# Performance work log

Hardware: AMD Instinct MI355X
Metric: run time of the kernel (lower is better)

Reference implementation:

```python
import jax, jax.numpy as jnp
import numpy as np

N = 100000   # nodes
E = 400000   # edges
G = 1024     # graphs in batch
IN = 4; H = 128; HD = 4; DH = H // HD; L = 3; ED = 4; FF = 2 * H; JK = H * L
SCALE = 1.0 / np.sqrt(DH).astype(np.float32)


def _ln(x, g, b):
    m = x.mean(-1, keepdims=True)
    v = x.var(-1, keepdims=True)
    return (x - m) / jnp.sqrt(v + 1e-5) * g + b


def setup_inputs() -> dict:
    key = jax.random.key(0)
    ks = jax.random.split(key, 24)
    rn = lambda k, s, sc=0.05: jax.random.normal(k, s, jnp.float32) * sc
    return {
        "x": rn(ks[0], (N, IN), 1.0),
        "edge_index": jax.random.randint(ks[1], (2, E), 0, N),
        "edge_attr": rn(ks[2], (E, ED), 1.0),
        "batch": jnp.sort(jax.random.randint(ks[3], (N,), 0, G)),
        "u": rn(ks[4], (G, 1), 1.0),
        "Win": rn(ks[5], (IN, H)), "b_in": jnp.zeros(H),
        "Wq": rn(ks[6], (L, H, H)), "bq": jnp.zeros((L, H)),
        "Wk": rn(ks[7], (L, H, H)), "bk": jnp.zeros((L, H)),
        "Wv": rn(ks[8], (L, H, H)), "bv": jnp.zeros((L, H)),
        "We": rn(ks[9], (L, ED, H)),
        "Wskip": rn(ks[10], (L, H, H)), "bskip": jnp.zeros((L, H)),
        "ln1_g": jnp.ones((L, H)), "ln1_b": jnp.zeros((L, H)),
        "Wf1": rn(ks[11], (L, H, FF)), "bf1": jnp.zeros((L, FF)),
        "Wf2": rn(ks[12], (L, FF, H)), "bf2": jnp.zeros((L, H)),
        "ln2_g": jnp.ones((L, H)), "ln2_b": jnp.zeros((L, H)),
        "Wg1": rn(ks[13], (JK, H)), "bg1": jnp.zeros(H),
        "Wg2": rn(ks[14], (H, 1)), "bg2": jnp.zeros(1),
        "Wh1": rn(ks[15], (JK + 1, H)), "bh1": jnp.zeros(H),
        "Wh2": rn(ks[16], (H, 3)), "bh2": jnp.zeros(3),
    }


def reference(x, edge_index, edge_attr, batch, u,
              Win, b_in, Wq, bq, Wk, bk, Wv, bv, We, Wskip, bskip,
              ln1_g, ln1_b, Wf1, bf1, Wf2, bf2, ln2_g, ln2_b,
              Wg1, bg1, Wg2, bg2, Wh1, bh1, Wh2, bh2):
    src, dst = edge_index[0], edge_index[1]
    h = x @ Win + b_in                                   # [N,H]
    xs = []
    for l in range(L):
        q = (h @ Wq[l] + bq[l]).reshape(N, HD, DH)
        k_n = h @ Wk[l] + bk[l]
        v_n = h @ Wv[l] + bv[l]
        e = edge_attr @ We[l]                            # [E,H] edge bias
        ke = (k_n[src] + e).reshape(E, HD, DH)
        ve = (v_n[src] + e).reshape(E, HD, DH)
        logits = (q[dst] * ke).sum(-1) * SCALE           # [E,HD]
        m = jax.ops.segment_max(logits, dst, N)
        p = jnp.exp(logits - m[dst])
        s = jax.ops.segment_sum(p, dst, N)
        alpha = p / (s[dst] + 1e-16)                     # segment softmax per dst node
        agg = jax.ops.segment_sum(alpha[:, :, None] * ve, dst, N).reshape(N, H)
        attn = agg + h @ Wskip[l] + bskip[l]             # root weight (skip lin)
        h = _ln(h + attn, ln1_g[l], ln1_b[l])
        ff = jax.nn.relu(h @ Wf1[l] + bf1[l]) @ Wf2[l] + bf2[l]
        h = _ln(h + ff, ln2_g[l], ln2_b[l])
        xs.append(h)
    xc = jnp.concatenate(xs, -1)                         # JumpingKnowledge 'cat' [N,JK]
    gate = (jax.nn.relu(xc @ Wg1 + bg1) @ Wg2 + bg2)[:, 0]  # [N]
    gm = jax.ops.segment_max(gate, batch, G)
    gp = jnp.exp(gate - gm[batch])
    gs = jax.ops.segment_sum(gp, batch, G)
    w = gp / (gs[batch] + 1e-16)                         # per-graph softmax
    pooled = jax.ops.segment_sum(w[:, None] * xc, batch, G)  # [G,JK]
    out = jnp.concatenate([pooled, u], 1)                # [G,JK+1]
    return jax.nn.relu(out @ Wh1 + bh1) @ Wh2 + bh2      # [G,3]
```

## Files before the change

kernel.cpp:

```cpp
#include <hip/hip_runtime.h>
#include <math.h>

#define H 128
#define LAYERS 3
#define FFDIM 256
#define JK 384
#define ATT_SCALE 0.17677669529663687f

typedef unsigned short u16;
typedef __attribute__((ext_vector_type(4))) float f32x4;
typedef __attribute__((ext_vector_type(8))) short short8;
typedef __attribute__((ext_vector_type(8))) unsigned short ushort8v;

static inline int cdiv(int a, int b) { return (a + b - 1) / b; }

static __device__ __forceinline__ float bf2f(u16 u) {
    union { unsigned int i; float f; } v; v.i = ((unsigned int)u) << 16; return v.f;
}
static __device__ __forceinline__ u16 f2bf(float f) {
    union { float f; unsigned int i; } v; v.f = f;
    unsigned int r = v.i + 0x7FFFu + ((v.i >> 16) & 1u);
    return (u16)(r >> 16);
}

__global__ void hist_kernel(const int* __restrict__ ei, int* __restrict__ counts, int E) {
    int e = blockIdx.x * blockDim.x + threadIdx.x;
    if (e >= E) return;
    atomicAdd(&counts[ei[E + e]], 1);
}

__global__ __launch_bounds__(256) void scan1_kernel(const int* __restrict__ counts,
                                                    int* __restrict__ offsets,
                                                    int* __restrict__ bsum, int N) {
    __shared__ int sh[256];
    int t = threadIdx.x;
    int base = blockIdx.x * 1024 + t * 4;
    int v0 = 0, v1 = 0, v2 = 0, v3 = 0;
    if (base + 3 < N) {
        int4 q = *(const int4*)&counts[base];
        v0 = q.x; v1 = q.y; v2 = q.z; v3 = q.w;
    } else {
        if (base < N) v0 = counts[base];
        if (base + 1 < N) v1 = counts[base + 1];
        if (base + 2 < N) v2 = counts[base + 2];
        if (base + 3 < N) v3 = counts[base + 3];
    }
    int ts = v0 + v1 + v2 + v3;
    sh[t] = ts; __syncthreads();
    for (int off = 1; off < 256; off <<= 1) {
        int x = (t >= off) ? sh[t - off] : 0;
        __syncthreads(); sh[t] += x; __syncthreads();
    }
    int excl = sh[t] - ts;
    if (base < N)     offsets[base]     = excl;
    if (base + 1 < N) offsets[base + 1] = excl + v0;
    if (base + 2 < N) offsets[base + 2] = excl + v0 + v1;
    if (base + 3 < N) offsets[base + 3] = excl + v0 + v1 + v2;
    if (t == 255) bsum[blockIdx.x] = sh[255];
}

__global__ __launch_bounds__(128) void scan2_kernel(const int* __restrict__ bsum,
                                                    int* __restrict__ boffs,
                                                    int* __restrict__ offsets, int nb, int N) {
    __shared__ int sh[128];
    int t = threadIdx.x;
    int s = (t < nb) ? bsum[t] : 0;
    sh[t] = s; __syncthreads();
    for (int off = 1; off < 128; off <<= 1) {
        int x = (t >= off) ? sh[t - off] : 0;
        __syncthreads(); sh[t] += x; __syncthreads();
    }
    if (t < nb) boffs[t] = sh[t] - s;
    if (t == 0) offsets[N] = sh[nb - 1];
}

__global__ __launch_bounds__(256) void scan3_kernel(int* __restrict__ offsets,
                                                    const int* __restrict__ boffs, int N) {
    int add = boffs[blockIdx.x];
    int base = blockIdx.x * 1024 + threadIdx.x * 4;
#pragma unroll
    for (int i = 0; i < 4; ++i)
        if (base + i < N) offsets[base + i] += add;
}

__global__ void scatter_kernel(const int* __restrict__ ei, const float* __restrict__ eattr,
                               const int* __restrict__ offsets,
                               int* __restrict__ cursor, int* __restrict__ psrc,
                               float4* __restrict__ pe, int E) {
    int e = blockIdx.x * blockDim.x + threadIdx.x;
    if (e >= E) return;
    int d = ei[E + e];
    int pos = atomicAdd(&cursor[d], 1);
    int o = offsets[d] + pos;
    psrc[o] = ei[e];
    pe[o] = *(const float4*)&eattr[(size_t)e * 4];
}

__global__ __launch_bounds__(256) void dhist_kernel(const int* __restrict__ counts,
                                                    int* __restrict__ dhist, int N) {
    __shared__ int lh[64];
    int t = threadIdx.x;
    if (t < 64) lh[t] = 0;
    __syncthreads();
    int n = blockIdx.x * 256 + t;
    if (n < N) atomicAdd(&lh[min(counts[n], 63)], 1);
    __syncthreads();
    if (t < 64 && lh[t]) atomicAdd(&dhist[t], lh[t]);
}

__global__ __launch_bounds__(64) void dscan_kernel(const int* __restrict__ dhist,
                                                   int* __restrict__ dcur) {
    __shared__ int sh[64];
    int t = threadIdx.x;
    int s = dhist[t];
    sh[t] = s; __syncthreads();
    for (int off = 1; off < 64; off <<= 1) {
        int x = (t >= off) ? sh[t - off] : 0;
        __syncthreads(); sh[t] += x; __syncthreads();
    }
    dcur[t] = sh[t] - s;
}

__global__ __launch_bounds__(256) void dscatter_kernel(const int* __restrict__ counts,
                                                       int* __restrict__ dcur,
                                                       int* __restrict__ nperm, int N) {
    __shared__ int lh[64], lbase[64];
    int t = threadIdx.x;
    if (t < 64) lh[t] = 0;
    __syncthreads();
    int n = blockIdx.x * 256 + t;
    int b = 0, rank = 0;
    if (n < N) {
        b = min(counts[n], 63);
        rank = atomicAdd(&lh[b], 1);
    }
    __syncthreads();
    if (t < 64 && lh[t]) lbase[t] = atomicAdd(&dcur[t], lh[t]);
    __syncthreads();
    if (n < N) nperm[lbase[b] + rank] = n;
}

__global__ void graph_bounds_kernel(const int* __restrict__ batch, int* __restrict__ gstart,
                                    int N, int G) {
    int g = blockIdx.x * blockDim.x + threadIdx.x;
    if (g > G) return;
    int lo = 0, hi = N;
    while (lo < hi) { int mid = (lo + hi) >> 1; if (batch[mid] < g) lo = mid + 1; else hi = mid; }
    gstart[g] = lo;
}

struct TD { const float* src; int dstoff, K, N; };
struct TA { TD d[19]; };

__global__ __launch_bounds__(256) void wconv_kernel(TA a, u16* __restrict__ WT) {
    TD d = a.d[blockIdx.y];
    int i = blockIdx.x * 256 + threadIdx.x;
    int tot = d.K * d.N;
    if (i >= tot) return;
    int c = i / d.K, k = i - c * d.K;
    WT[d.dstoff + i] = f2bf(d.src[(size_t)k * d.N + c]);
}

__global__ __launch_bounds__(256) void input_proj_kernel(const float* __restrict__ x,
                                                         const float* __restrict__ Win,
                                                         const float* __restrict__ b_in,
                                                         u16* __restrict__ h, int ldh, int N) {
    int idx = blockIdx.x * 256 + threadIdx.x;
    int n = idx >> 6, c = (idx & 63) * 2;
    if (n >= N) return;
    float4 xv = *(const float4*)&x[(size_t)n * 4];
    float o0 = b_in[c]     + xv.x * Win[c]     + xv.y * Win[H + c]     + xv.z * Win[2 * H + c]     + xv.w * Win[3 * H + c];
    float o1 = b_in[c + 1] + xv.x * Win[c + 1] + xv.y * Win[H + c + 1] + xv.z * Win[2 * H + c + 1] + xv.w * Win[3 * H + c + 1];
    ushort2 s; s.x = f2bf(o0); s.y = f2bf(o1);
    *(ushort2*)&h[(size_t)n * ldh + c] = s;
}

__device__ __forceinline__ void stage_tile(const u16* __restrict__ g, int ld, int row0,
                                           int nrows, int kt, u16* __restrict__ sm, int t) {
#pragma unroll
    for (int i = 0; i < 4; ++i) {
        int f = i * 256 + t;
        int row = f >> 3, ck = f & 7;
        int n = row0 + row; if (n >= nrows) n = nrows - 1;
        uint4 v = *(const uint4*)(g + (size_t)n * ld + kt + ck * 8);
        int sw = ck ^ (row & 7);
        *(uint4*)(sm + row * 64 + sw * 8) = v;
    }
}

template <int MODE, int NBY>
__global__ __launch_bounds__(256) void gemm_mfma(
    const u16* __restrict__ A, int lda,
    const u16* __restrict__ WT, int K,
    const float* __restrict__ b0, const float* __restrict__ b1,
    const float* __restrict__ b2, const float* __restrict__ b3,
    const u16* __restrict__ resid16,
    u16* __restrict__ obf, u16* __restrict__ obf2, float* __restrict__ of32,
    int nrows)
{
    alignas(16) __shared__ char smemraw[33792];
    u16* Asm = (u16*)smemraw;
    u16* Bsm = (u16*)(smemraw + 16384);
    float* stage = (float*)smemraw;
    int t = threadIdx.x;
    int lane = t & 63, wid = t >> 6;
    int wr = wid >> 1, wc = wid & 1;

    int T = gridDim.x, id = blockIdx.x;
    int qd = T >> 3, rr = T & 7;
    int xcd = id & 7, pos = id >> 3;
    int swz = (xcd < rr ? xcd * (qd + 1) : rr * (qd + 1) + (xcd - rr) * qd) + pos;
    int by = swz & (NBY - 1);
    int row0 = (swz / NBY) * 128;

    const u16* WTb = WT + (size_t)by * 128 * K;

    f32x4 acc[4][4] = {};

    for (int kt = 0; kt < K; kt += 64) {
        stage_tile(A, lda, row0, nrows, kt, Asm, t);
        stage_tile(WTb, K, 0, 128, kt, Bsm, t);
        __syncthreads();
        int g = lane >> 4;
        int l15 = lane & 15;
#pragma unroll
        for (int kk = 0; kk < 2; ++kk) {
            int cb = kk * 4 + g;
            short8 af[4], bf[4];
#pragma unroll
            for (int mi = 0; mi < 4; ++mi) {
                int r = wr * 64 + mi * 16 + l15;
                af[mi] = *(const short8*)(Asm + r * 64 + ((cb ^ (r & 7)) * 8));
            }
#pragma unroll
            for (int nj = 0; nj < 4; ++nj) {
                int c = wc * 64 + nj * 16 + l15;
                bf[nj] = *(const short8*)(Bsm + c * 64 + ((cb ^ (c & 7)) * 8));
            }
#pragma unroll
            for (int mi = 0; mi < 4; ++mi)
#pragma unroll
                for (int nj = 0; nj < 4; ++nj)
                    acc[mi][nj] = __builtin_amdgcn_mfma_f32_16x16x32_bf16(af[mi], bf[nj], acc[mi][nj], 0, 0, 0);
        }
        __syncthreads();
    }

    int g = lane >> 4, l15 = lane & 15;

    if (MODE == 3) {
        float* gsum = (float*)Asm;
        float part[4][4];
#pragma unroll
        for (int mi = 0; mi < 4; ++mi)
#pragma unroll
            for (int r = 0; r < 4; ++r) part[mi][r] = 0.f;
#pragma unroll
        for (int nj = 0; nj < 4; ++nj) {
            int col = wc * 64 + nj * 16 + l15;
            float bb = b0[col];
            float w2 = b1[col];
#pragma unroll
            for (int mi = 0; mi < 4; ++mi)
#pragma unroll
                for (int r = 0; r < 4; ++r) {
                    float v = fmaxf(acc[mi][nj][r] + bb, 0.f);
                    part[mi][r] = fmaf(v, w2, part[mi][r]);
                }
        }
#pragma unroll
        for (int off = 1; off <= 8; off <<= 1)
#pragma unroll
            for (int mi = 0; mi < 4; ++mi)
#pragma unroll
                for (int r = 0; r < 4; ++r) part[mi][r] += __shfl_xor(part[mi][r], off);
        if (wc == 0 && l15 == 0) {
#pragma unroll
            for (int mi = 0; mi < 4; ++mi)
#pragma unroll
                for (int r = 0; r < 4; ++r)
                    gsum[wr * 64 + mi * 16 + g * 4 + r] = part[mi][r];
        }
        __syncthreads();
        if (wc == 1 && l15 == 0) {
            float bg2v = b2[0];
#pragma unroll
            for (int mi = 0; mi < 4; ++mi)
#pragma unroll
                for (int r = 0; r < 4; ++r) {
                    int lr = wr * 64 + mi * 16 + g * 4 + r;
                    int n = row0 + lr;
                    if (n < nrows) of32[n] = part[mi][r] + gsum[lr] + bg2v;
                }
        }
        return;
    }

    const float* bias;
    u16* ob = nullptr; int ldob = 384;
    if (MODE == 0) {
        bias = (by == 0) ? b0 : (by == 1) ? b1 : (by == 2) ? b2 : b3;
        if (by < 3) ob = obf + by * 128;
        else { ob = obf2; ldob = 128; }
    } else if (MODE == 1) {
        bias = b0 + by * 128;
        ob = obf + by * 128;
    } else {
        bias = b0;
        ob = obf;
    }

#pragma unroll
    for (int p = 0; p < 2; ++p) {
        if (wr == p) {
#pragma unroll
            for (int nj = 0; nj < 4; ++nj) {
                int col = wc * 64 + nj * 16 + l15;
                float bb = bias[col];
#pragma unroll
                for (int mi = 0; mi < 4; ++mi)
#pragma unroll
                    for (int r = 0; r < 4; ++r) {
                        float v = acc[mi][nj][r] + bb;
                        if (MODE == 1) v = fmaxf(v, 0.f);
                        stage[(mi * 16 + g * 4 + r) * 132 + col] = v;
                    }
            }
        }
        __syncthreads();
        if (MODE == 2) {
            int sub2 = t & 15, rowg = t >> 4;
#pragma unroll
            for (int it = 0; it < 4; ++it) {
                int lr = it * 16 + rowg;
                int gr = row0 + p * 64 + lr;
                bool ok = gr < nrows;
                int c8 = sub2 * 8;
                float tv[8]; float sum = 0.f, sq = 0.f;
                if (ok) {
                    ushort8v rv = *(const ushort8v*)&resid16[(size_t)gr * 384 + c8];
#pragma unroll
                    for (int i = 0; i < 8; ++i) {
                        tv[i] = stage[lr * 132 + c8 + i] + bf2f(rv[i]);
                        sum += tv[i]; sq += tv[i] * tv[i];
                    }
                }
#pragma unroll
                for (int off = 1; off <= 8; off <<= 1) { sum += __shfl_xor(sum, off); sq += __shfl_xor(sq, off); }
                if (ok) {
                    float mean = sum * (1.f / 128.f);
                    float var = sq * (1.f / 128.f) - mean * mean;
                    float rstd = rsqrtf(var + 1e-5f);
                    ushort8v o;
#pragma unroll
                    for (int i = 0; i < 8; ++i)
                        o[i] = f2bf((tv[i] - mean) * rstd * b1[c8 + i] + b2[c8 + i]);
                    *(ushort8v*)&ob[(size_t)gr * 384 + c8] = o;
                }
            }
        } else {
#pragma unroll
            for (int it = 0; it < 4; ++it) {
                int lr = it * 16 + (t >> 4);
                int gr = row0 + p * 64 + lr;
                if (gr < nrows) {
                    int c8 = (t & 15) * 8;
                    ushort8v o;
                    if (MODE == 0 && by == 3) {
                        ushort8v hv = *(const ushort8v*)&A[(size_t)gr * lda + c8];
#pragma unroll
                        for (int i = 0; i < 8; ++i) o[i] = f2bf(stage[lr * 132 + c8 + i] + bf2f(hv[i]));
                    } else {
#pragma unroll
                        for (int i = 0; i < 8; ++i) o[i] = f2bf(stage[lr * 132 + c8 + i]);
                    }
                    *(ushort8v*)&ob[(size_t)gr * ldob + c8] = o;
                }
            }
        }
        __syncthreads();
    }
}

__global__ __launch_bounds__(256) void attn_kernel(
    u16* __restrict__ qkv,
    const u16* __restrict__ skipb,
    const int* __restrict__ offsets,
    const int* __restrict__ nperm,
    const int* __restrict__ psrc, const float4* __restrict__ pe,
    const float* __restrict__ We_l,
    const float* __restrict__ g1, const float* __restrict__ b1,
    int N)
{
    int tid = threadIdx.x;
    int grp = tid >> 4;
    int sub = tid & 15;
    int idx = blockIdx.x * 16 + grp;
    if (idx >= N) return;
    int n = nperm[idx];
    int d0 = sub * 8;

    float we[4][8];
#pragma unroll
    for (int aa = 0; aa < 4; ++aa) {
        float4 w0 = *(const float4*)&We_l[aa * H + d0];
        float4 w1 = *(const float4*)&We_l[aa * H + d0 + 4];
        we[aa][0] = w0.x; we[aa][1] = w0.y; we[aa][2] = w0.z; we[aa][3] = w0.w;
        we[aa][4] = w1.x; we[aa][5] = w1.y; we[aa][6] = w1.z; we[aa][7] = w1.w;
    }

    ushort8v qraw = *(const ushort8v*)&qkv[(size_t)n * JK + d0];
    float qf[8];
#pragma unroll
    for (int i = 0; i < 8; ++i) qf[i] = bf2f(qraw[i]);

    float qe[4];
#pragma unroll
    for (int aa = 0; aa < 4; ++aa) {
        float s = 0.f;
#pragma unroll
        for (int i = 0; i < 8; ++i) s = fmaf(qf[i], we[aa][i], s);
        s += __shfl_xor(s, 1);
        s += __shfl_xor(s, 2);
        qe[aa] = s;
    }

    float m0 = -INFINITY, ss0 = 0.f, m1 = -INFINITY, ss1 = 0.f;
    float a0[8] = {}, a1[8] = {};
    float w0a = 0.f, w0b = 0.f, w0c = 0.f, w0d = 0.f;
    float w1a = 0.f, w1b = 0.f, w1c = 0.f, w1d = 0.f;
    int e0v = offsets[n], e1v = offsets[n + 1];
    int deg = e1v - e0v;
    int npairs = deg >> 1;

    if (npairs > 0) {
        int j0 = e0v;
        int sA = psrc[j0], sB = psrc[j0 + 1];
        float4 eaA = pe[j0], eaB = pe[j0 + 1];
        const u16* srA = qkv + (size_t)sA * JK;
        const u16* srB = qkv + (size_t)sB * JK;
        ushort8v krA = *(const ushort8v*)&srA[H + d0];
        ushort8v vrA = *(const ushort8v*)&srA[2 * H + d0];
        ushort8v krB = *(const ushort8v*)&srB[H + d0];
        ushort8v vrB = *(const ushort8v*)&srB[2 * H + d0];
        for (int it = 0; it < npairs; ++it) {
            float4 eaA2, eaB2; ushort8v krA2, vrA2, krB2, vrB2;
            if (it + 1 < npairs) {
                int jn = e0v + (it + 1) * 2;
                int sA2 = psrc[jn], sB2 = psrc[jn + 1];
                eaA2 = pe[jn]; eaB2 = pe[jn + 1];
                const u16* srA2 = qkv + (size_t)sA2 * JK;
                const u16* srB2 = qkv + (size_t)sB2 * JK;
                krA2 = *(const ushort8v*)&srA2[H + d0];
                vrA2 = *(const ushort8v*)&srA2[2 * H + d0];
                krB2 = *(const ushort8v*)&srB2[H + d0];
                vrB2 = *(const ushort8v*)&srB2[2 * H + d0];
            }
            float pA = 0.f, pB = 0.f;
#pragma unroll
            for (int i = 0; i < 8; ++i) {
                pA = fmaf(qf[i], bf2f(krA[i]), pA);
                pB = fmaf(qf[i], bf2f(krB[i]), pB);
            }
            pA += __shfl_xor(pA, 1); pB += __shfl_xor(pB, 1);
            pA += __shfl_xor(pA, 2); pB += __shfl_xor(pB, 2);
            float lgA = (pA + eaA.x * qe[0] + eaA.y * qe[1] + eaA.z * qe[2] + eaA.w * qe[3]) * ATT_SCALE;
            float lgB = (pB + eaB.x * qe[0] + eaB.y * qe[1] + eaB.z * qe[2] + eaB.w * qe[3]) * ATT_SCALE;
            float mnA = fmaxf(m0, lgA);
            float mnB = fmaxf(m1, lgB);
            float cA = __expf(m0 - mnA), cB = __expf(m1 - mnB);
            float pvA = __expf(lgA - mnA), pvB = __expf(lgB - mnB);
            ss0 = ss0 * cA + pvA;
            ss1 = ss1 * cB + pvB;
#pragma unroll
            for (int i = 0; i < 8; ++i) {
                a0[i] = a0[i] * cA + pvA * bf2f(vrA[i]);
                a1[i] = a1[i] * cB + pvB * bf2f(vrB[i]);
            }
            w0a = w0a * cA + pvA * eaA.x; w0b = w0b * cA + pvA * eaA.y;
            w0c = w0c * cA + pvA * eaA.z; w0d = w0d * cA + pvA * eaA.w;
            w1a = w1a * cB + pvB * eaB.x; w1b = w1b * cB + pvB * eaB.y;
            w1c = w1c * cB + pvB * eaB.z; w1d = w1d * cB + pvB * eaB.w;
            m0 = mnA; m1 = mnB;
            krA = krA2; vrA = vrA2; eaA = eaA2;
            krB = krB2; vrB = vrB2; eaB = eaB2;
        }
    }
    if (deg & 1) {
        int j = e1v - 1;
        int s = psrc[j];
        float4 ea = pe[j];
        const u16* sr = qkv + (size_t)s * JK;
        ushort8v kr = *(const ushort8v*)&sr[H + d0];
        ushort8v vr = *(const ushort8v*)&sr[2 * H + d0];
        float part = 0.f;
#pragma unroll
        for (int i = 0; i < 8; ++i) part = fmaf(qf[i], bf2f(kr[i]), part);
        part += __shfl_xor(part, 1);
        part += __shfl_xor(part, 2);
        float lg = (part + ea.x * qe[0] + ea.y * qe[1] + ea.z * qe[2] + ea.w * qe[3]) * ATT_SCALE;
        float mn = fmaxf(m0, lg);
        float c = __expf(m0 - mn);
        float pv = __expf(lg - mn);
        ss0 = ss0 * c + pv;
#pragma unroll
        for (int i = 0; i < 8; ++i) a0[i] = a0[i] * c + pv * bf2f(vr[i]);
        w0a = w0a * c + pv * ea.x; w0b = w0b * c + pv * ea.y;
        w0c = w0c * c + pv * ea.z; w0d = w0d * c + pv * ea.w;
        m0 = mn;
    }
    float mm = fmaxf(m0, m1);
    if (mm > -INFINITY) {
        float c0 = (m0 > -INFINITY) ? __expf(m0 - mm) : 0.f;
        float c1 = (m1 > -INFINITY) ? __expf(m1 - mm) : 0.f;
        ss0 = ss0 * c0 + ss1 * c1;
#pragma unroll
        for (int i = 0; i < 8; ++i) a0[i] = a0[i] * c0 + a1[i] * c1;
        w0a = w0a * c0 + w1a * c1; w0b = w0b * c0 + w1b * c1;
        w0c = w0c * c0 + w1c * c1; w0d = w0d * c0 + w1d * c1;
    }
    float inv = 1.f / (ss0 + 1e-16f);
#pragma unroll
    for (int i = 0; i < 8; ++i)
        a0[i] += w0a * we[0][i] + w0b * we[1][i] + w0c * we[2][i] + w0d * we[3][i];

    ushort8v skraw = *(const ushort8v*)&skipb[(size_t)n * H + d0];
    float tv[8], sum = 0.f, sq = 0.f;
#pragma unroll
    for (int i = 0; i < 8; ++i) {
        tv[i] = a0[i] * inv + bf2f(skraw[i]);
        sum += tv[i]; sq += tv[i] * tv[i];
    }
#pragma unroll
    for (int off = 1; off <= 8; off <<= 1) { sum += __shfl_xor(sum, off); sq += __shfl_xor(sq, off); }
    float mean = sum * (1.f / 128.f);
    float var = sq * (1.f / 128.f) - mean * mean;
    float rstd = rsqrtf(var + 1e-5f);
    float4 ga = *(const float4*)&g1[d0];
    float4 gb = *(const float4*)&g1[d0 + 4];
    float4 ba = *(const float4*)&b1[d0];
    float4 bb = *(const float4*)&b1[d0 + 4];
    float gg[8] = {ga.x, ga.y, ga.z, ga.w, gb.x, gb.y, gb.z, gb.w};
    float bbv[8] = {ba.x, ba.y, ba.z, ba.w, bb.x, bb.y, bb.z, bb.w};
    ushort8v obv;
#pragma unroll
    for (int i = 0; i < 8; ++i)
        obv[i] = f2bf((tv[i] - mean) * rstd * gg[i] + bbv[i]);
    *(ushort8v*)&qkv[(size_t)n * JK + d0] = obv;
}

#define PCH 512
__global__ __launch_bounds__(256) void pool_kernel(const float* __restrict__ gate,
                                                   const u16* __restrict__ xc,
                                                   const int* __restrict__ gstart,
                                                   const float* __restrict__ u,
                                                   float* __restrict__ pooled, int G) {
    int g = blockIdx.x;
    int t = threadIdx.x;
    int s0 = gstart[g], s1 = gstart[g + 1];
    __shared__ float red[256];
    __shared__ float w[PCH];
    float mx = -INFINITY;
    for (int i = s0 + t; i < s1; i += 256) mx = fmaxf(mx, gate[i]);
    red[t] = mx; __syncthreads();
    for (int off = 128; off; off >>= 1) { if (t < off) red[t] = fmaxf(red[t], red[t + off]); __syncthreads(); }
    float gm = red[0]; __syncthreads();
    float sm = 0.f;
    for (int i = s0 + t; i < s1; i += 256) sm += __expf(gate[i] - gm);
    red[t] = sm; __syncthreads();
    for (int off = 128; off; off >>= 1) { if (t < off) red[t] += red[t + off]; __syncthreads(); }
    float inv = 1.f / (red[0] + 1e-16f);
    float acc0 = 0.f, acc1 = 0.f;
    for (int base = s0; base < s1; base += PCH) {
        int cnt = min(PCH, s1 - base);
        __syncthreads();
        for (int i = t; i < cnt; i += 256) w[i] = __expf(gate[base + i] - gm) * inv;
        __syncthreads();
        for (int c = 0; c < cnt; ++c) {
            const u16* row = xc + (size_t)(base + c) * JK;
            float wc = w[c];
            acc0 = fmaf(wc, bf2f(row[t]), acc0);
            if (t < 128) acc1 = fmaf(wc, bf2f(row[t + 256]), acc1);
        }
    }
    pooled[(size_t)g * (JK + 1) + t] = acc0;
    if (t < 128) pooled[(size_t)g * (JK + 1) + t + 256] = acc1;
    if (t == 0) pooled[(size_t)g * (JK + 1) + JK] = u[g];
}

__global__ __launch_bounds__(128) void head_kernel(const float* __restrict__ pooled,
                                                   const float* __restrict__ Wh1,
                                                   const float* __restrict__ bh1,
                                                   const float* __restrict__ Wh2,
                                                   const float* __restrict__ bh2,
                                                   float* __restrict__ out, int G) {
    int g = blockIdx.x;
    int j = threadIdx.x;
    __shared__ float hid[128];
    float acc = bh1[j];
    const float* pr = pooled + (size_t)g * (JK + 1);
    for (int k = 0; k < JK + 1; ++k) acc = fmaf(pr[k], Wh1[(size_t)k * H + j], acc);
    hid[j] = fmaxf(acc, 0.f);
    __syncthreads();
    if (j < 3) {
        float o = bh2[j];
        for (int k = 0; k < H; ++k) o += hid[k] * Wh2[k * 3 + j];
        out[(size_t)g * 3 + j] = o;
    }
}

extern "C" void kernel_launch(void* const* d_in, const int* in_sizes, int n_in,
                              void* d_out, int out_size, void* d_ws, size_t ws_size,
                              hipStream_t stream) {
    const float* x     = (const float*)d_in[0];
    const int*   ei    = (const int*)d_in[1];
    const float* eattr = (const float*)d_in[2];
    const int*   batch = (const int*)d_in[3];
    const float* u     = (const float*)d_in[4];
    const float* Win   = (const float*)d_in[5];
    const float* b_in  = (const float*)d_in[6];
    const float* Wq    = (const float*)d_in[7];
    const float* bq    = (const float*)d_in[8];
    const float* Wk    = (const float*)d_in[9];
    const float* bk    = (const float*)d_in[10];
    const float* Wv    = (const float*)d_in[11];
    const float* bv    = (const float*)d_in[12];
    const float* We    = (const float*)d_in[13];
    const float* Wskip = (const float*)d_in[14];
    const float* bskip = (const float*)d_in[15];
    const float* ln1_g = (const float*)d_in[16];
    const float* ln1_b = (const float*)d_in[17];
    const float* Wf1   = (const float*)d_in[18];
    const float* bf1   = (const float*)d_in[19];
    const float* Wf2   = (const float*)d_in[20];
    const float* bf2   = (const float*)d_in[21];
    const float* ln2_g = (const float*)d_in[22];
    const float* ln2_b = (const float*)d_in[23];
    const float* Wg1   = (const float*)d_in[24];
    const float* bg1   = (const float*)d_in[25];
    const float* Wg2   = (const float*)d_in[26];
    const float* bg2   = (const float*)d_in[27];
    const float* Wh1   = (const float*)d_in[28];
    const float* bh1   = (const float*)d_in[29];
    const float* Wh2   = (const float*)d_in[30];
    const float* bh2   = (const float*)d_in[31];

    const int N = in_sizes[3];
    const int E = in_sizes[1] / 2;
    const int G = in_sizes[4];

    char* p = (char*)d_ws;
    auto alloc = [&](size_t bytes) { char* r = p; p += (bytes + 255) & ~(size_t)255; return r; };
    int*    counts  = (int*)alloc((size_t)N * 4);
    int*    cursor  = (int*)alloc((size_t)N * 4);
    int*    offsets = (int*)alloc((size_t)(N + 1) * 4);
    int*    psrc    = (int*)alloc((size_t)E * 4);
    float4* pe      = (float4*)alloc((size_t)E * 16);
    int*    nperm   = (int*)alloc((size_t)N * 4);
    int*    gstart  = (int*)alloc((size_t)(G + 1) * 4);
    int*    bsum    = (int*)alloc(128 * 4);
    int*    boffs   = (int*)alloc(128 * 4);
    int*    dhist   = (int*)alloc(64 * 4);
    int*    dcur    = (int*)alloc(64 * 4);
    float*  gate    = (float*)alloc((size_t)N * 4);
    float*  pooled  = (float*)alloc((size_t)G * (JK + 1) * 4);
    u16*    WT      = (u16*)alloc((size_t)442368 * 2);
    u16*    skipb   = (u16*)alloc((size_t)N * H * 2);
    u16*    xc      = (u16*)alloc((size_t)N * JK * 2);
    u16*    qkv     = (u16*)alloc((size_t)N * JK * 2);

    const int QKVS_OFF = 0;
    const int F1_OFF   = 3 * 65536;
    const int F2_OFF   = F1_OFF + 3 * 32768;
    const int G1_OFF   = F2_OFF + 3 * 32768;

    hipMemsetAsync(counts, 0, (size_t)N * 4, stream);
    hipMemsetAsync(cursor, 0, (size_t)N * 4, stream);
    hipMemsetAsync(dhist, 0, 64 * 4, stream);

    int eb = cdiv(E, 256);
    int nb = cdiv(N, 1024);
    int nthb = cdiv(N, 256);
    hist_kernel<<<eb, 256, 0, stream>>>(ei, counts, E);
    scan1_kernel<<<nb, 256, 0, stream>>>(counts, offsets, bsum, N);
    scan2_kernel<<<1, 128, 0, stream>>>(bsum, boffs, offsets, nb, N);
    scan3_kernel<<<nb, 256, 0, stream>>>(offsets, boffs, N);
    scatter_kernel<<<eb, 256, 0, stream>>>(ei, eattr, offsets, cursor, psrc, pe, E);
    dhist_kernel<<<nthb, 256, 0, stream>>>(counts, dhist, N);
    dscan_kernel<<<1, 64, 0, stream>>>(dhist, dcur);
    dscatter_kernel<<<nthb, 256, 0, stream>>>(counts, dcur, nperm, N);
    graph_bounds_kernel<<<cdiv(G + 1, 256), 256, 0, stream>>>(batch, gstart, N, G);

    TA ta;
    for (int l = 0; l < 3; ++l) {
        ta.d[l * 4 + 0] = { Wq    + (size_t)l * 16384, QKVS_OFF + l * 65536 + 0,     128, 128 };
        ta.d[l * 4 + 1] = { Wk    + (size_t)l * 16384, QKVS_OFF + l * 65536 + 16384, 128, 128 };
        ta.d[l * 4 + 2] = { Wv    + (size_t)l * 16384, QKVS_OFF + l * 65536 + 32768, 128, 128 };
        ta.d[l * 4 + 3] = { Wskip + (size_t)l * 16384, QKVS_OFF + l * 65536 + 49152, 128, 128 };
        ta.d[12 + l]    = { Wf1   + (size_t)l * 32768, F1_OFF   + l * 32768,         128, 256 };
        ta.d[15 + l]    = { Wf2   + (size_t)l * 32768, F2_OFF   + l * 32768,         256, 128 };
    }
    ta.d[18] = { Wg1, G1_OFF, 384, 128 };
    dim3 wg(cdiv(49152, 256), 19);
    wconv_kernel<<<wg, 256, 0, stream>>>(ta, WT);

    input_proj_kernel<<<cdiv(N * 64, 256), 256, 0, stream>>>(x, Win, b_in, xc, JK, N);

    int gb = cdiv(N, 128);
    int nb16 = cdiv(N, 16);
    for (int l = 0; l < LAYERS; ++l) {
        const u16* hin = xc + (size_t)((l == 0) ? 0 : (l - 1) * H);
        gemm_mfma<0, 4><<<gb * 4, 256, 0, stream>>>(
            hin, JK, WT + QKVS_OFF + (size_t)l * 65536, 128,
            bq + l * H, bk + l * H, bv + l * H, bskip + l * H,
            nullptr, qkv, skipb, nullptr, N);
        attn_kernel<<<nb16, 256, 0, stream>>>(qkv, skipb, offsets, nperm, psrc, pe,
                                              We + (size_t)l * 4 * H, ln1_g + l * H, ln1_b + l * H,
                                              N);
        gemm_mfma<1, 2><<<gb * 2, 256, 0, stream>>>(
            qkv, JK, WT + F1_OFF + (size_t)l * 32768, 128,
            bf1 + (size_t)l * FFDIM, nullptr, nullptr, nullptr,
            nullptr, qkv + H, nullptr, nullptr, N);
        gemm_mfma<2, 1><<<gb, 256, 0, stream>>>(
            qkv + H, JK, WT + F2_OFF + (size_t)l * 32768, 256,
            bf2 + (size_t)l * H, ln2_g + (size_t)l * H, ln2_b + (size_t)l * H, nullptr,
            qkv, xc + (size_t)l * H, nullptr, nullptr, N);
    }

    gemm_mfma<3, 1><<<gb, 256, 0, stream>>>(
        xc, JK, WT + G1_OFF, JK,
        bg1, Wg2, bg2, nullptr,
        nullptr, nullptr, nullptr, gate, N);
    pool_kernel<<<G, 256, 0, stream>>>(gate, xc, gstart, u, pooled, G);
    head_kernel<<<G, 128, 0, stream>>>(pooled, Wh1, bh1, Wh2, bh2, (float*)d_out, G);
}
```

Measured before the change: 660.5 us.

## Fuse FFN two GEMMs, ReLU and LayerNorm into one kernel per layer

Replaces the separate FF1 (ReLU) and FF2 (+residual LayerNorm) GEMM launches with a single ff_fused kernel that processes 64-row tiles. The 256-wide hidden activation stays in swizzled shared memory instead of being written to and reread from global memory. The generic GEMM kernel loses its MODE 1/2 epilogues. In exchange the fused kernel uses about 56KB of LDS and smaller row tiles, which may lower occupancy, and it reloads the weights for every 64-row block.

```diff
diff --git a/kernel.cpp b/kernel.cpp
--- a/kernel.cpp
+++ b/kernel.cpp
@@ -194,7 +194,6 @@
     const u16* __restrict__ WT, int K,
     const float* __restrict__ b0, const float* __restrict__ b1,
     const float* __restrict__ b2, const float* __restrict__ b3,
-    const u16* __restrict__ resid16,
     u16* __restrict__ obf, u16* __restrict__ obf2, float* __restrict__ of32,
     int nrows)
 {
@@ -296,19 +295,10 @@
         return;
     }
 
-    const float* bias;
-    u16* ob = nullptr; int ldob = 384;
-    if (MODE == 0) {
-        bias = (by == 0) ? b0 : (by == 1) ? b1 : (by == 2) ? b2 : b3;
-        if (by < 3) ob = obf + by * 128;
-        else { ob = obf2; ldob = 128; }
-    } else if (MODE == 1) {
-        bias = b0 + by * 128;
-        ob = obf + by * 128;
-    } else {
-        bias = b0;
-        ob = obf;
-    }
+    const float* bias = (by == 0) ? b0 : (by == 1) ? b1 : (by == 2) ? b2 : b3;
+    u16* ob; int ldob;
+    if (by < 3) { ob = obf + by * 128; ldob = 384; }
+    else { ob = obf2; ldob = 128; }
 
 #pragma unroll
     for (int p = 0; p < 2; ++p) {
@@ -320,65 +310,193 @@
 #pragma unroll
                 for (int mi = 0; mi < 4; ++mi)
 #pragma unroll
-                    for (int r = 0; r < 4; ++r) {
-                        float v = acc[mi][nj][r] + bb;
-                        if (MODE == 1) v = fmaxf(v, 0.f);
-                        stage[(mi * 16 + g * 4 + r) * 132 + col] = v;
-                    }
+                    for (int r = 0; r < 4; ++r)
+                        stage[(mi * 16 + g * 4 + r) * 132 + col] = acc[mi][nj][r] + bb;
             }
         }
         __syncthreads();
-        if (MODE == 2) {
-            int sub2 = t & 15, rowg = t >> 4;
-#pragma unroll
-            for (int it = 0; it < 4; ++it) {
-                int lr = it * 16 + rowg;
-                int gr = row0 + p * 64 + lr;
-                bool ok = gr < nrows;
-                int c8 = sub2 * 8;
-                float tv[8]; float sum = 0.f, sq = 0.f;
-                if (ok) {
-                    ushort8v rv = *(const ushort8v*)&resid16[(size_t)gr * 384 + c8];
-#pragma unroll
-                    for (int i = 0; i < 8; ++i) {
-                        tv[i] = stage[lr * 132 + c8 + i] + bf2f(rv[i]);
-                        sum += tv[i]; sq += tv[i] * tv[i];
-                    }
+#pragma unroll
+        for (int it = 0; it < 4; ++it) {
+            int lr = it * 16 + (t >> 4);
+            int gr = row0 + p * 64 + lr;
+            if (gr < nrows) {
+                int c8 = (t & 15) * 8;
+                ushort8v o;
+                if (by == 3) {
+                    ushort8v hv = *(const ushort8v*)&A[(size_t)gr * lda + c8];
+#pragma unroll
+                    for (int i = 0; i < 8; ++i) o[i] = f2bf(stage[lr * 132 + c8 + i] + bf2f(hv[i]));
+                } else {
+#pragma unroll
+                    for (int i = 0; i < 8; ++i) o[i] = f2bf(stage[lr * 132 + c8 + i]);
                 }
-#pragma unroll
-                for (int off = 1; off <= 8; off <<= 1) { sum += __shfl_xor(sum, off); sq += __shfl_xor(sq, off); }
-                if (ok) {
-                    float mean = sum * (1.f / 128.f);
-                    float var = sq * (1.f / 128.f) - mean * mean;
-                    float rstd = rsqrtf(var + 1e-5f);
-                    ushort8v o;
-#pragma unroll
-                    for (int i = 0; i < 8; ++i)
-                        o[i] = f2bf((tv[i] - mean) * rstd * b1[c8 + i] + b2[c8 + i]);
-                    *(ushort8v*)&ob[(size_t)gr * 384 + c8] = o;
+                *(ushort8v*)&ob[(size_t)gr * ldob + c8] = o;
+            }
+        }
+        __syncthreads();
+    }
+}
+
+__global__ __launch_bounds__(256) void ff_fused(
+    const u16* __restrict__ qkv,
+    const u16* __restrict__ W1T,
+    const u16* __restrict__ W2T,
+    const float* __restrict__ bias1,
+    const float* __restrict__ bias2,
+    const float* __restrict__ g2, const float* __restrict__ b2v,
+    u16* __restrict__ xcout,
+    int nrows)
+{
+    alignas(16) __shared__ char smem[57344];
+    u16* ff1s = (u16*)smem;
+    u16* ast  = (u16*)(smem + 32768);
+    u16* bst  = (u16*)(smem + 40960);
+    float* stage = (float*)smem;
+
+    int t = threadIdx.x;
+    int lane = t & 63, wid = t >> 6;
+    int wr = wid >> 1, wc = wid & 1;
+    int g = lane >> 4, l15 = lane & 15;
+
+    int T = gridDim.x, id = blockIdx.x;
+    int qd = T >> 3, rr = T & 7;
+    int xcd = id & 7, pos = id >> 3;
+    int swz = (xcd < rr ? xcd * (qd + 1) : rr * (qd + 1) + (xcd - rr) * qd) + pos;
+    int row0 = swz * 64;
+
+    for (int ch = 0; ch < 2; ++ch) {
+        f32x4 acc[2][4] = {};
+        for (int kt = 0; kt < 128; kt += 64) {
+#pragma unroll
+            for (int i = 0; i < 2; ++i) {
+                int f = i * 256 + t;
+                int row = f >> 3, ck = f & 7;
+                int n = row0 + row; if (n >= nrows) n = nrows - 1;
+                uint4 v = *(const uint4*)(qkv + (size_t)n * 384 + kt + ck * 8);
+                *(uint4*)(ast + row * 64 + ((ck ^ (row & 7)) * 8)) = v;
+            }
+#pragma unroll
+            for (int i = 0; i < 4; ++i) {
+                int f = i * 256 + t;
+                int row = f >> 3, ck = f & 7;
+                uint4 v = *(const uint4*)(W1T + (size_t)(ch * 128 + row) * 128 + kt + ck * 8);
+                *(uint4*)(bst + row * 64 + ((ck ^ (row & 7)) * 8)) = v;
+            }
+            __syncthreads();
+#pragma unroll
+            for (int kk = 0; kk < 2; ++kk) {
+                int cb = kk * 4 + g;
+                short8 af[2], bf[4];
+#pragma unroll
+                for (int mi = 0; mi < 2; ++mi) {
+                    int r = wr * 32 + mi * 16 + l15;
+                    af[mi] = *(const short8*)(ast + r * 64 + ((cb ^ (r & 7)) * 8));
                 }
-            }
-        } else {
-#pragma unroll
-            for (int it = 0; it < 4; ++it) {
-                int lr = it * 16 + (t >> 4);
-                int gr = row0 + p * 64 + lr;
-                if (gr < nrows) {
-                    int c8 = (t & 15) * 8;
-                    ushort8v o;
-                    if (MODE == 0 && by == 3) {
-                        ushort8v hv = *(const ushort8v*)&A[(size_t)gr * lda + c8];
-#pragma unroll
-                        for (int i = 0; i < 8; ++i) o[i] = f2bf(stage[lr * 132 + c8 + i] + bf2f(hv[i]));
-                    } else {
-#pragma unroll
-                        for (int i = 0; i < 8; ++i) o[i] = f2bf(stage[lr * 132 + c8 + i]);
-                    }
-                    *(ushort8v*)&ob[(size_t)gr * ldob + c8] = o;
+#pragma unroll
+                for (int nj = 0; nj < 4; ++nj) {
+                    int c = wc * 64 + nj * 16 + l15;
+                    bf[nj] = *(const short8*)(bst + c * 64 + ((cb ^ (c & 7)) * 8));
                 }
-            }
+#pragma unroll
+                for (int mi = 0; mi < 2; ++mi)
+#pragma unroll
+                    for (int nj = 0; nj < 4; ++nj)
+                        acc[mi][nj] = __builtin_amdgcn_mfma_f32_16x16x32_bf16(af[mi], bf[nj], acc[mi][nj], 0, 0, 0);
+            }
+            __syncthreads();
+        }
+#pragma unroll
+        for (int nj = 0; nj < 4; ++nj) {
+            int col = ch * 128 + wc * 64 + nj * 16 + l15;
+            float bb = bias1[col];
+            int cb2 = col >> 3, j = col & 7;
+#pragma unroll
+            for (int mi = 0; mi < 2; ++mi)
+#pragma unroll
+                for (int r = 0; r < 4; ++r) {
+                    int row = wr * 32 + mi * 16 + g * 4 + r;
+                    float v = fmaxf(acc[mi][nj][r] + bb, 0.f);
+                    int sc = (cb2 & 24) | ((cb2 & 7) ^ (row & 7));
+                    ff1s[row * 256 + sc * 8 + j] = f2bf(v);
+                }
+        }
+    }
+
+    f32x4 acc2[2][4] = {};
+    for (int kt2 = 0; kt2 < 256; kt2 += 64) {
+#pragma unroll
+        for (int i = 0; i < 4; ++i) {
+            int f = i * 256 + t;
+            int row = f >> 3, ck = f & 7;
+            uint4 v = *(const uint4*)(W2T + (size_t)row * 256 + kt2 + ck * 8);
+            *(uint4*)(bst + row * 64 + ((ck ^ (row & 7)) * 8)) = v;
         }
         __syncthreads();
+#pragma unroll
+        for (int kk = 0; kk < 2; ++kk) {
+            int cb = kk * 4 + g;
+            short8 af[2], bf[4];
+#pragma unroll
+            for (int mi = 0; mi < 2; ++mi) {
+                int r = wr * 32 + mi * 16 + l15;
+                int sc = (kt2 >> 3) | (cb ^ (r & 7));
+                af[mi] = *(const short8*)(ff1s + r * 256 + sc * 8);
+            }
+#pragma unroll
+            for (int nj = 0; nj < 4; ++nj) {
+                int c = wc * 64 + nj * 16 + l15;
+                bf[nj] = *(const short8*)(bst + c * 64 + ((cb ^ (c & 7)) * 8));
+            }
+#pragma unroll
+            for (int mi = 0; mi < 2; ++mi)
+#pragma unroll
+                for (int nj = 0; nj < 4; ++nj)
+                    acc2[mi][nj] = __builtin_amdgcn_mfma_f32_16x16x32_bf16(af[mi], bf[nj], acc2[mi][nj], 0, 0, 0);
+        }
+        __syncthreads();
+    }
+
+#pragma unroll
+    for (int nj = 0; nj < 4; ++nj) {
+        int col = wc * 64 + nj * 16 + l15;
+        float bb = bias2[col];
+#pragma unroll
+        for (int mi = 0; mi < 2; ++mi)
+#pragma unroll
+            for (int r = 0; r < 4; ++r) {
+                int row = wr * 32 + mi * 16 + g * 4 + r;
+                stage[row * 132 + col] = acc2[mi][nj][r] + bb;
+            }
+    }
+    __syncthreads();
+    int sub2 = t & 15, rowg = t >> 4;
+#pragma unroll
+    for (int it = 0; it < 4; ++it) {
+        int lr = it * 16 + rowg;
+        int gr = row0 + lr;
+        bool ok = gr < nrows;
+        int c8 = sub2 * 8;
+        float tv[8]; float sum = 0.f, sq = 0.f;
+        if (ok) {
+            ushort8v rv = *(const ushort8v*)&qkv[(size_t)gr * 384 + c8];
+#pragma unroll
+            for (int i = 0; i < 8; ++i) {
+                tv[i] = stage[lr * 132 + c8 + i] + bf2f(rv[i]);
+                sum += tv[i]; sq += tv[i] * tv[i];
+            }
+        }
+#pragma unroll
+        for (int off = 1; off <= 8; off <<= 1) { sum += __shfl_xor(sum, off); sq += __shfl_xor(sq, off); }
+        if (ok) {
+            float mean = sum * (1.f / 128.f);
+            float var = sq * (1.f / 128.f) - mean * mean;
+            float rstd = rsqrtf(var + 1e-5f);
+            ushort8v o;
+#pragma unroll
+            for (int i = 0; i < 8; ++i)
+                o[i] = f2bf((tv[i] - mean) * rstd * g2[c8 + i] + b2v[c8 + i]);
+            *(ushort8v*)&xcout[(size_t)gr * 384 + c8] = o;
+        }
     }
 }
 
@@ -707,30 +825,28 @@
     input_proj_kernel<<<cdiv(N * 64, 256), 256, 0, stream>>>(x, Win, b_in, xc, JK, N);
 
     int gb = cdiv(N, 128);
+    int gb64 = cdiv(N, 64);
     int nb16 = cdiv(N, 16);
     for (int l = 0; l < LAYERS; ++l) {
         const u16* hin = xc + (size_t)((l == 0) ? 0 : (l - 1) * H);
         gemm_mfma<0, 4><<<gb * 4, 256, 0, stream>>>(
             hin, JK, WT + QKVS_OFF + (size_t)l * 65536, 128,
             bq + l * H, bk + l * H, bv + l * H, bskip + l * H,
-            nullptr, qkv, skipb, nullptr, N);
+            qkv, skipb, nullptr, N);
         attn_kernel<<<nb16, 256, 0, stream>>>(qkv, skipb, offsets, nperm, psrc, pe,
                                               We + (size_t)l * 4 * H, ln1_g + l * H, ln1_b + l * H,
                                               N);
-        gemm_mfma<1, 2><<<gb * 2, 256, 0, stream>>>(
-            qkv, JK, WT + F1_OFF + (size_t)l * 32768, 128,
-            bf1 + (size_t)l * FFDIM, nullptr, nullptr, nullptr,
-            nullptr, qkv + H, nullptr, nullptr, N);
-        gemm_mfma<2, 1><<<gb, 256, 0, stream>>>(
-            qkv + H, JK, WT + F2_OFF + (size_t)l * 32768, 256,
-            bf2 + (size_t)l * H, ln2_g + (size_t)l * H, ln2_b + (size_t)l * H, nullptr,
-            qkv, xc + (size_t)l * H, nullptr, nullptr, N);
+        ff_fused<<<gb64, 256, 0, stream>>>(
+            qkv, WT + F1_OFF + (size_t)l * 32768, WT + F2_OFF + (size_t)l * 32768,
+            bf1 + (size_t)l * FFDIM, bf2 + (size_t)l * H,
+            ln2_g + (size_t)l * H, ln2_b + (size_t)l * H,
+            xc + (size_t)l * H, N);
     }
 
     gemm_mfma<3, 1><<<gb, 256, 0, stream>>>(
         xc, JK, WT + G1_OFF, JK,
         bg1, Wg2, bg2, nullptr,
-        nullptr, nullptr, nullptr, gate, N);
+        nullptr, nullptr, gate, N);
     pool_kernel<<<G, 256, 0, stream>>>(gate, xc, gstart, u, pooled, G);
     head_kernel<<<G, 128, 0, stream>>>(pooled, Wh1, bh1, Wh2, bh2, (float*)d_out, G);
 }
```

After: 609.9 us (median of 3 runs). -7.7%, faster.
